# Kernel tuning notes

Hardware: AMD Instinct MI355X
Metric: run time of the kernel (lower is better)

The kernel has to match this reference:

```python
import jax, jax.numpy as jnp
import numpy as np

N = 1048576
HID = 64
GEO = 15


def _glorot(key, in_dim, out_dim):
    # torch nn.Linear default init: U(-1/sqrt(in), 1/sqrt(in)); stored here as [in, out]
    bound = 1.0 / np.sqrt(in_dim)
    return jax.random.uniform(key, (in_dim, out_dim), jnp.float32, -bound, bound)


def setup_inputs() -> dict:
    key = jax.random.key(0)
    ks = jax.random.split(key, 8)
    x = jax.random.normal(ks[0], (N, 6), dtype=jnp.float32)
    # sigma_net: 3 -> 64 -> 64 -> (1 + geo_feat_dim)=16, no bias
    ws0 = _glorot(ks[1], 3, HID)
    ws1 = _glorot(ks[2], HID, HID)
    ws2 = _glorot(ks[3], HID, 1 + GEO)
    # color_net: (3 + 15)=18 -> 64 -> 64 -> 3, no bias
    wc0 = _glorot(ks[4], 3 + GEO, HID)
    wc1 = _glorot(ks[5], HID, HID)
    wc2 = _glorot(ks[6], HID, HID)
    wc3 = _glorot(ks[7], HID, 3)
    return {"x": x, "ws0": ws0, "ws1": ws1, "ws2": ws2,
            "wc0": wc0, "wc1": wc1, "wc2": wc2, "wc3": wc3}


def reference(x, ws0, ws1, ws2, wc0, wc1, wc2, wc3):
    input_pts, input_views = x[..., :3], x[..., 3:]
    # sigma net: Linear+ReLU x2, final Linear
    h = jax.nn.relu(input_pts @ ws0)
    h = jax.nn.relu(h @ ws1)
    h = h @ ws2                       # [N, 16]
    sigma = jax.nn.softplus(h[..., 0])  # [N]
    geo_feat = h[..., 1:]               # [N, 15]
    # color net
    c = jnp.concatenate([input_views, geo_feat], axis=-1)  # [N, 18]
    c = jax.nn.relu(c @ wc0)
    c = jax.nn.relu(c @ wc1)
    c = jax.nn.relu(c @ wc2)
    color = c @ wc3                    # [N, 3]
    return jnp.concatenate([color, sigma[..., None]], axis=-1)  # [N, 4]
```

## Files before the change

kernel.cpp:

```cpp
#include <hip/hip_runtime.h>
#include <math.h>
#include <stdint.h>

typedef short bf16x8 __attribute__((ext_vector_type(8)));
typedef float f32x4 __attribute__((ext_vector_type(4)));

#define NFRAGS 36
#define T 4
#define NW 8
#define BS (NW * 64)
#define PTS_BLK (NW * T * 16)

__device__ __forceinline__ uint32_t f2bf_rne(float f) {
    uint32_t u = __float_as_uint(f);
    return (u + 0x7FFFu + ((u >> 16) & 1u)) >> 16;
}

__device__ __forceinline__ uint32_t pk2(float a, float b) {
    return __builtin_amdgcn_perm(__float_as_uint(b), __float_as_uint(a), 0x07060302u);
}
__device__ __forceinline__ uint32_t relu2(uint32_t x) {
    uint32_t r;
    asm("v_pk_max_i16 %0, %1, 0" : "=v"(r) : "v"(x));
    return r;
}
__device__ __forceinline__ uint32_t pk2r(float a, float b) { return relu2(pk2(a, b)); }
__device__ __forceinline__ uint16_t bfu(float v) { return (uint16_t)(__float_as_uint(v) >> 16); }

__device__ __forceinline__ int sperm(int k) {
    return (k & 3) | (((k >> 2) & 3) << 4) | (((k >> 4) & 3) << 2);
}
__device__ __forceinline__ int rperm(int k) {
    return (k & 32) | (((k >> 3) & 1) << 4) | (((k >> 4) & 1) << 3) | (k & 7);
}

__global__ void pack_weights(const float* __restrict__ ws0, const float* __restrict__ ws1,
                             const float* __restrict__ ws2, const float* __restrict__ wc0,
                             const float* __restrict__ wc1, const float* __restrict__ wc2,
                             const float* __restrict__ wc3, uint4* __restrict__ wpack) {
    int idx = blockIdx.x * blockDim.x + threadIdx.x;
    if (idx >= NFRAGS * 64) return;
    int F = idx >> 6, cl = idx & 63, cm = cl & 15, cq = cl >> 4;
    const float* w; int IN, OUT, mt, ks, pm;
    if (F < 4)       { w = ws0; IN = 3;  OUT = 64; mt = F;            ks = 0;          pm = 0; }
    else if (F < 12) { w = ws1; IN = 64; OUT = 64; mt = (F-4) >> 1;   ks = (F-4) & 1;  pm = 2; }
    else if (F < 14) { w = ws2; IN = 64; OUT = 16; mt = 0;            ks = F - 12;     pm = 2; }
    else if (F < 18) { w = wc0; IN = 18; OUT = 64; mt = F - 14;       ks = 0;          pm = 0; }
    else if (F < 26) { w = wc1; IN = 64; OUT = 64; mt = (F-18) >> 1;  ks = (F-18) & 1; pm = 2; }
    else if (F < 34) { w = wc2; IN = 64; OUT = 64; mt = (F-26) >> 1;  ks = (F-26) & 1; pm = 2; }
    else             { w = wc3; IN = 64; OUT = 3;  mt = 0;            ks = F - 34;     pm = 2; }
    const int fo = mt * 16 + cm;
    uint32_t pk[4];
    for (int jj = 0; jj < 4; ++jj) {
        uint32_t h[2];
        for (int bb = 0; bb < 2; ++bb) {
            int kg = ks * 32 + cq * 8 + jj * 2 + bb;
            int kr = (pm == 2) ? sperm(rperm(kg)) : kg;
            float v = 0.f;
            if (fo < OUT && kr < IN) v = w[kr * OUT + fo];
            h[bb] = f2bf_rne(v);
        }
        pk[jj] = h[0] | (h[1] << 16);
    }
    wpack[F * 64 + cl] = make_uint4(pk[0], pk[1], pk[2], pk[3]);
}

__global__ __launch_bounds__(BS, 4) void nerf_main(const float* __restrict__ xin,
                                                   const uint4* __restrict__ wpack,
                                                   float* __restrict__ outp, int n) {
    __shared__ __align__(16) char smem[NW * T * 1024];
    const int tid = threadIdx.x, wv = tid >> 6, lane = tid & 63;
    const int p = lane & 15, q = lane >> 4;
    const int sw = p & 7;
    char* actw = smem + wv * (T * 1024);
    const int base = blockIdx.x * PTS_BLK + wv * (T * 16);

    auto aaddr = [&](int t, int g) -> char* {
        return actw + (t >> 1) * 2048 + p * 128 + (((g ^ ((t & 1) << 2)) ^ sw) << 4);
    };
    auto ldA = [&](int F) -> bf16x8 {
        uint4 u = wpack[F * 64 + lane];
        return *(bf16x8*)&u;
    };
    const f32x4 z4 = {0.f, 0.f, 0.f, 0.f};

    auto xpose = [&](const f32x4* d, bf16x8& b0, bf16x8& b1) {
        uint32_t X0 = pk2r(d[0][0], d[0][1]), X1 = pk2r(d[0][2], d[0][3]);
        uint32_t X2 = pk2r(d[1][0], d[1][1]), X3 = pk2r(d[1][2], d[1][3]);
        uint32_t X4 = pk2r(d[2][0], d[2][1]), X5 = pk2r(d[2][2], d[2][3]);
        uint32_t X6 = pk2r(d[3][0], d[3][1]), X7 = pk2r(d[3][2], d[3][3]);
        asm("v_permlane32_swap_b32 %0, %1" : "+v"(X0), "+v"(X4));
        asm("v_permlane32_swap_b32 %0, %1" : "+v"(X1), "+v"(X5));
        asm("v_permlane32_swap_b32 %0, %1" : "+v"(X2), "+v"(X6));
        asm("v_permlane32_swap_b32 %0, %1" : "+v"(X3), "+v"(X7));
        uint4 u0 = make_uint4(X0, X1, X2, X3), u1 = make_uint4(X4, X5, X6, X7);
        b0 = *(bf16x8*)&u0; b1 = *(bf16x8*)&u1;
    };

    float vv0 = 0.f, vv1 = 0.f, vv2 = 0.f;
    {
        float x0 = 0.f, x1 = 0.f, x2 = 0.f;
        const int pi = base + q * 16 + p;
        if (pi < n) {
            const float2* xp = (const float2*)(xin + (size_t)pi * 6);
            float2 a = xp[0], b = xp[1], c = xp[2];
            x0 = a.x; x1 = a.y; x2 = b.x; vv0 = b.y; vv1 = c.x; vv2 = c.y;
        }
        *(uint4*)aaddr(q, 0) = make_uint4(pk2(x0, x1), pk2(x2, 0.f), 0u, 0u);
    }

    bf16x8 c0[T], c1[T];

    auto layerK32 = [&](int FB, int qmax) {
        bf16x8 W0 = ldA(FB), W1 = ldA(FB + 1), W2 = ldA(FB + 2), W3 = ldA(FB + 3);
#pragma unroll
        for (int t = 0; t < T; ++t) {
            bf16x8 b = 0;
            if (q < qmax) b = *(const bf16x8*)aaddr(t, q);
            f32x4 d[4];
            d[0] = __builtin_amdgcn_mfma_f32_16x16x32_bf16(W0, b, z4, 0, 0, 0);
            d[1] = __builtin_amdgcn_mfma_f32_16x16x32_bf16(W1, b, z4, 0, 0, 0);
            d[2] = __builtin_amdgcn_mfma_f32_16x16x32_bf16(W2, b, z4, 0, 0, 0);
            d[3] = __builtin_amdgcn_mfma_f32_16x16x32_bf16(W3, b, z4, 0, 0, 0);
            xpose(d, c0[t], c1[t]);
        }
    };

    auto layer64 = [&](int FB) {
        bf16x8 W[8];
#pragma unroll
        for (int i = 0; i < 8; ++i) W[i] = ldA(FB + i);
#pragma unroll
        for (int t = 0; t < T; ++t) {
            f32x4 d[4];
            __builtin_amdgcn_s_setprio(1);
#pragma unroll
            for (int mt = 0; mt < 4; ++mt) {
                f32x4 acc = __builtin_amdgcn_mfma_f32_16x16x32_bf16(W[mt*2],   c0[t], z4,  0, 0, 0);
                d[mt]     = __builtin_amdgcn_mfma_f32_16x16x32_bf16(W[mt*2+1], c1[t], acc, 0, 0, 0);
            }
            __builtin_amdgcn_s_setprio(0);
            xpose(d, c0[t], c1[t]);
        }
    };

    layerK32(0, 1);

    layer64(4);

    float sig[T];
    {
        bf16x8 A0 = ldA(12), A1 = ldA(13);
#pragma unroll
        for (int t = 0; t < T; ++t) {
            f32x4 acc = __builtin_amdgcn_mfma_f32_16x16x32_bf16(A0, c0[t], z4,  0, 0, 0);
            f32x4 d   = __builtin_amdgcn_mfma_f32_16x16x32_bf16(A1, c1[t], acc, 0, 0, 0);
            const float sx = d[0];
            sig[t] = fmaxf(sx, 0.f) + __logf(1.f + __expf(-fabsf(sx)));
            if (q == 2) *(uint4*)aaddr(t, 2) = make_uint4(0u, 0u, 0u, 0u);
            if (q == t) {
                *(uint32_t*)(aaddr(t, 0) + 0) = pk2(vv0, vv1);
                *(uint16_t*)(aaddr(t, 0) + 4) = bfu(vv2);
            }
            if (q == 0) {
                *(uint16_t*)(aaddr(t, 0) + 6) = bfu(d[1]);
                *(uint32_t*)(aaddr(t, 0) + 8) = pk2(d[2], d[3]);
            } else if (q == 1) {
                *(uint32_t*)(aaddr(t, 0) + 12) = pk2(d[0], d[1]);
                *(uint32_t*)(aaddr(t, 1) + 0)  = pk2(d[2], d[3]);
            } else if (q == 2) {
                *(uint32_t*)(aaddr(t, 1) + 4) = pk2(d[0], d[1]);
                *(uint32_t*)(aaddr(t, 1) + 8) = pk2(d[2], d[3]);
            } else {
                *(uint32_t*)(aaddr(t, 1) + 12) = pk2(d[0], d[1]);
                *(uint32_t*)(aaddr(t, 2) + 0)  = pk2(d[2], d[3]);
            }
        }
    }

    layerK32(14, 3);

    layer64(18);
    layer64(26);

    {
        bf16x8 A0 = ldA(34), A1 = ldA(35);
#pragma unroll
        for (int t = 0; t < T; ++t) {
            f32x4 acc = __builtin_amdgcn_mfma_f32_16x16x32_bf16(A0, c0[t], z4,  0, 0, 0);
            f32x4 d   = __builtin_amdgcn_mfma_f32_16x16x32_bf16(A1, c1[t], acc, 0, 0, 0);
            if (q == 0) {
                const int pt = base + t * 16 + p;
                if (pt < n)
                    *(float4*)(outp + (size_t)pt * 4) = make_float4(d[0], d[1], d[2], sig[t]);
            }
        }
    }
}

extern "C" void kernel_launch(void* const* d_in, const int* in_sizes, int n_in,
                              void* d_out, int out_size, void* d_ws, size_t ws_size,
                              hipStream_t stream) {
    const float* x   = (const float*)d_in[0];
    const float* ws0 = (const float*)d_in[1];
    const float* ws1 = (const float*)d_in[2];
    const float* ws2 = (const float*)d_in[3];
    const float* wc0 = (const float*)d_in[4];
    const float* wc1 = (const float*)d_in[5];
    const float* wc2 = (const float*)d_in[6];
    const float* wc3 = (const float*)d_in[7];
    float* out = (float*)d_out;
    uint4* wpack = (uint4*)d_ws;

    const int n = in_sizes[0] / 6;
    pack_weights<<<(NFRAGS * 64 + 255) / 256, 256, 0, stream>>>(ws0, ws1, ws2, wc0, wc1, wc2, wc3, wpack);
    const int grid = (n + PTS_BLK - 1) / PTS_BLK;
    nerf_main<<<grid, BS, 0, stream>>>(x, wpack, out, n);
}
```

Before: 118.4 us.

## Prefetch weight fragments with inline asm loads and explicit vmcnt waits; shrink block to 4 waves

Replaces per-layer weight fragment loads with hand-issued global_load_dwordx4 instructions. Each layer's weights are fetched one or more layers ahead, and waits are explicit vmcnt counters, so weight latency overlaps with MFMA work of earlier layers. Block size also drops from 8 waves to 4, giving smaller blocks and more of them. This raises register pressure because many weight fragments stay live at once, and the hand-counted waits are fragile if the compiler emits other memory operations that also count toward vmcnt.

```diff
diff --git a/kernel.cpp b/kernel.cpp
--- a/kernel.cpp
+++ b/kernel.cpp
@@ -7,8 +7,8 @@
 
 #define NFRAGS 36
 #define T 4
-#define NW 8
-#define BS (NW * 64)
+#define NW 4
+#define BS 256
 #define PTS_BLK (NW * T * 16)
 
 __device__ __forceinline__ uint32_t f2bf_rne(float f) {
@@ -65,6 +65,12 @@
     wpack[F * 64 + cl] = make_uint4(pk[0], pk[1], pk[2], pk[3]);
 }
 
+#define GLD(dst, base, off) \
+    asm volatile("global_load_dwordx4 %0, %1, %2 offset:" #off \
+                 : "=v"(dst) : "v"(voff), "s"(base))
+#define VMW(N) do { asm volatile("s_waitcnt vmcnt(" #N ")" ::: "memory"); \
+                    __builtin_amdgcn_sched_barrier(0); } while (0)
+
 __global__ __launch_bounds__(BS, 4) void nerf_main(const float* __restrict__ xin,
                                                    const uint4* __restrict__ wpack,
                                                    float* __restrict__ outp, int n) {
@@ -77,10 +83,6 @@
 
     auto aaddr = [&](int t, int g) -> char* {
         return actw + (t >> 1) * 2048 + p * 128 + (((g ^ ((t & 1) << 2)) ^ sw) << 4);
-    };
-    auto ldA = [&](int F) -> bf16x8 {
-        uint4 u = wpack[F * 64 + lane];
-        return *(bf16x8*)&u;
     };
     const f32x4 z4 = {0.f, 0.f, 0.f, 0.f};
 
@@ -111,25 +113,21 @@
 
     bf16x8 c0[T], c1[T];
 
-    auto layerK32 = [&](int FB, int qmax) {
-        bf16x8 W0 = ldA(FB), W1 = ldA(FB + 1), W2 = ldA(FB + 2), W3 = ldA(FB + 3);
+    auto layerK32 = [&](const bf16x8 (&W)[4], int qmax) {
 #pragma unroll
         for (int t = 0; t < T; ++t) {
             bf16x8 b = 0;
             if (q < qmax) b = *(const bf16x8*)aaddr(t, q);
             f32x4 d[4];
-            d[0] = __builtin_amdgcn_mfma_f32_16x16x32_bf16(W0, b, z4, 0, 0, 0);
-            d[1] = __builtin_amdgcn_mfma_f32_16x16x32_bf16(W1, b, z4, 0, 0, 0);
-            d[2] = __builtin_amdgcn_mfma_f32_16x16x32_bf16(W2, b, z4, 0, 0, 0);
-            d[3] = __builtin_amdgcn_mfma_f32_16x16x32_bf16(W3, b, z4, 0, 0, 0);
+            d[0] = __builtin_amdgcn_mfma_f32_16x16x32_bf16(W[0], b, z4, 0, 0, 0);
+            d[1] = __builtin_amdgcn_mfma_f32_16x16x32_bf16(W[1], b, z4, 0, 0, 0);
+            d[2] = __builtin_amdgcn_mfma_f32_16x16x32_bf16(W[2], b, z4, 0, 0, 0);
+            d[3] = __builtin_amdgcn_mfma_f32_16x16x32_bf16(W[3], b, z4, 0, 0, 0);
             xpose(d, c0[t], c1[t]);
         }
     };
 
-    auto layer64 = [&](int FB) {
-        bf16x8 W[8];
-#pragma unroll
-        for (int i = 0; i < 8; ++i) W[i] = ldA(FB + i);
+    auto layer64 = [&](const bf16x8 (&W)[8]) {
 #pragma unroll
         for (int t = 0; t < T; ++t) {
             f32x4 d[4];
@@ -144,17 +142,34 @@
         }
     };
 
-    layerK32(0, 1);
-
-    layer64(4);
-
+    const uint32_t voff = (uint32_t)lane * 16u;
+    const uint4 *b0p = wpack,            *b4p = wpack + 4*64,  *b8p = wpack + 8*64;
+    const uint4 *b12p = wpack + 12*64,   *b14p = wpack + 14*64;
+    const uint4 *b18p = wpack + 18*64,   *b22p = wpack + 22*64;
+    const uint4 *b26p = wpack + 26*64,   *b30p = wpack + 30*64, *b34p = wpack + 34*64;
+
+    bf16x8 LA[4], LB[8];
+    GLD(LA[0], b0p, 0); GLD(LA[1], b0p, 1024); GLD(LA[2], b0p, 2048); GLD(LA[3], b0p, 3072);
+    GLD(LB[0], b4p, 0); GLD(LB[1], b4p, 1024); GLD(LB[2], b4p, 2048); GLD(LB[3], b4p, 3072);
+    GLD(LB[4], b8p, 0); GLD(LB[5], b8p, 1024); GLD(LB[6], b8p, 2048); GLD(LB[7], b8p, 3072);
+
+    VMW(8);
+    layerK32(LA, 1);
+    bf16x8 LC[2];
+    GLD(LC[0], b12p, 0); GLD(LC[1], b12p, 1024);
+
+    VMW(2);
+    layer64(LB);
+    bf16x8 LD[4];
+    GLD(LD[0], b14p, 0); GLD(LD[1], b14p, 1024); GLD(LD[2], b14p, 2048); GLD(LD[3], b14p, 3072);
+
+    VMW(4);
     float sig[T];
     {
-        bf16x8 A0 = ldA(12), A1 = ldA(13);
-#pragma unroll
-        for (int t = 0; t < T; ++t) {
-            f32x4 acc = __builtin_amdgcn_mfma_f32_16x16x32_bf16(A0, c0[t], z4,  0, 0, 0);
-            f32x4 d   = __builtin_amdgcn_mfma_f32_16x16x32_bf16(A1, c1[t], acc, 0, 0, 0);
+#pragma unroll
+        for (int t = 0; t < T; ++t) {
+            f32x4 acc = __builtin_amdgcn_mfma_f32_16x16x32_bf16(LC[0], c0[t], z4,  0, 0, 0);
+            f32x4 d   = __builtin_amdgcn_mfma_f32_16x16x32_bf16(LC[1], c1[t], acc, 0, 0, 0);
             const float sx = d[0];
             sig[t] = fmaxf(sx, 0.f) + __logf(1.f + __expf(-fabsf(sx)));
             if (q == 2) *(uint4*)aaddr(t, 2) = make_uint4(0u, 0u, 0u, 0u);
@@ -177,18 +192,29 @@
             }
         }
     }
-
-    layerK32(14, 3);
-
-    layer64(18);
-    layer64(26);
-
+    bf16x8 LE[8], LF[8];
+    GLD(LE[0], b18p, 0); GLD(LE[1], b18p, 1024); GLD(LE[2], b18p, 2048); GLD(LE[3], b18p, 3072);
+    GLD(LE[4], b22p, 0); GLD(LE[5], b22p, 1024); GLD(LE[6], b22p, 2048); GLD(LE[7], b22p, 3072);
+    GLD(LF[0], b26p, 0); GLD(LF[1], b26p, 1024); GLD(LF[2], b26p, 2048); GLD(LF[3], b26p, 3072);
+
+    VMW(12);
+    layerK32(LD, 3);
+    GLD(LF[4], b30p, 0); GLD(LF[5], b30p, 1024); GLD(LF[6], b30p, 2048); GLD(LF[7], b30p, 3072);
+    bf16x8 LG[2];
+    GLD(LG[0], b34p, 0); GLD(LG[1], b34p, 1024);
+
+    VMW(10);
+    layer64(LE);
+
+    VMW(2);
+    layer64(LF);
+
+    VMW(0);
     {
-        bf16x8 A0 = ldA(34), A1 = ldA(35);
-#pragma unroll
-        for (int t = 0; t < T; ++t) {
-            f32x4 acc = __builtin_amdgcn_mfma_f32_16x16x32_bf16(A0, c0[t], z4,  0, 0, 0);
-            f32x4 d   = __builtin_amdgcn_mfma_f32_16x16x32_bf16(A1, c1[t], acc, 0, 0, 0);
+#pragma unroll
+        for (int t = 0; t < T; ++t) {
+            f32x4 acc = __builtin_amdgcn_mfma_f32_16x16x32_bf16(LG[0], c0[t], z4,  0, 0, 0);
+            f32x4 d   = __builtin_amdgcn_mfma_f32_16x16x32_bf16(LG[1], c1[t], acc, 0, 0, 0);
             if (q == 0) {
                 const int pt = base + t * 16 + p;
                 if (pt < n)
```

Measured after the change: 115.3 us. -2.6%, faster.
